# Kernel optimization log

Measured on AMD Instinct MI355X. Metric: run time of the kernel, lower is better.

The kernel has to match this reference:

```python
import jax, jax.numpy as jnp
import numpy as np

N = 4096      # nodes
E = 131072    # edges
C_IN = 128
HID = 128     # d_model of transformer (= embed_dim used in reshape_to_trans)
OUT = 32      # GNN output channels -> transformer seq_len
HEADS = 8
DH = HID // HEADS
FF = 2048     # torch TransformerEncoderLayer default dim_feedforward
EPS = 1e-5


def layer_norm(x, g, b):
    mu = jnp.mean(x, axis=-1, keepdims=True)
    var = jnp.mean(jnp.square(x - mu), axis=-1, keepdims=True)
    return (x - mu) * jax.lax.rsqrt(var + EPS) * g + b


def setup_inputs() -> dict:
    key = jax.random.key(0)
    ks = jax.random.split(key, 24)
    def rn(k, shape, scale=0.05):
        return jax.random.normal(k, shape, dtype=jnp.float32) * scale
    inp = {
        "x": jax.random.normal(ks[0], (N, C_IN), dtype=jnp.float32),
        "edge_index": jax.random.randint(ks[1], (2, E), 0, N, dtype=jnp.int64),
        # GCN layers
        "Wg1": rn(ks[2], (C_IN, HID)), "bg1": jnp.zeros((HID,), jnp.float32),
        "Wg2": rn(ks[3], (HID, HID)),  "bg2": jnp.zeros((HID,), jnp.float32),
        "Wg3": rn(ks[4], (HID, OUT)),  "bg3": jnp.zeros((OUT,), jnp.float32),
        # MHA
        "Wq": rn(ks[5], (HID, HID)), "bq": jnp.zeros((HID,), jnp.float32),
        "Wk": rn(ks[6], (HID, HID)), "bk": jnp.zeros((HID,), jnp.float32),
        "Wv": rn(ks[7], (HID, HID)), "bv": jnp.zeros((HID,), jnp.float32),
        "Wo": rn(ks[8], (HID, HID)), "bo": jnp.zeros((HID,), jnp.float32),
        "ln1_g": jnp.ones((HID,), jnp.float32), "ln1_b": jnp.zeros((HID,), jnp.float32),
        # FFN
        "W1": rn(ks[9], (HID, FF)),  "b1": jnp.zeros((FF,), jnp.float32),
        "W2": rn(ks[10], (FF, HID)), "b2": jnp.zeros((HID,), jnp.float32),
        "ln2_g": jnp.ones((HID,), jnp.float32), "ln2_b": jnp.zeros((HID,), jnp.float32),
    }
    return inp


def reference(x, edge_index, Wg1, bg1, Wg2, bg2, Wg3, bg3,
              Wq, bq, Wk, bk, Wv, bv, Wo, bo, ln1_g, ln1_b,
              W1, b1, W2, b2, ln2_g, ln2_b):
    # ---- GCN normalization (add self-loops, symmetric D^-1/2 (A+I) D^-1/2) ----
    loop = jnp.arange(N, dtype=edge_index.dtype)
    src = jnp.concatenate([edge_index[0], loop])
    dst = jnp.concatenate([edge_index[1], loop])
    deg = jax.ops.segment_sum(jnp.ones((E + N,), jnp.float32), dst, num_segments=N)
    dinv = jnp.where(deg > 0, jax.lax.rsqrt(deg), 0.0)
    norm = (dinv[src] * dinv[dst])[:, None]  # [E+N, 1]

    def gcn(h, W, b):
        m = h @ W                               # [N, d_out]
        agg = jax.ops.segment_sum(m[src] * norm, dst, num_segments=N)
        return agg + b

    h = jax.nn.relu(gcn(x, Wg1, bg1))
    h = jax.nn.relu(gcn(h, Wg2, bg2))
    h = jax.nn.relu(gcn(h, Wg3, bg3))           # [N, OUT]

    # ---- reshape_to_trans: [N, OUT] -> [N, OUT, HID] (repeat along embed dim) ----
    t = jnp.broadcast_to(h[:, :, None], (N, OUT, HID))

    # ---- TransformerEncoderLayer (post-norm, relu FFN, no dropout at eval) ----
    q = (t @ Wq + bq).reshape(N, OUT, HEADS, DH)
    k = (t @ Wk + bk).reshape(N, OUT, HEADS, DH)
    v = (t @ Wv + bv).reshape(N, OUT, HEADS, DH)
    scores = jnp.einsum("bqhd,bkhd->bhqk", q, k) / jnp.sqrt(jnp.float32(DH))
    attn = jax.nn.softmax(scores, axis=-1)
    ctx = jnp.einsum("bhqk,bkhd->bqhd", attn, v).reshape(N, OUT, HID)
    a = ctx @ Wo + bo
    x1 = layer_norm(t + a, ln1_g, ln1_b)
    f = jax.nn.relu(x1 @ W1 + b1) @ W2 + b2
    out = layer_norm(x1 + f, ln2_g, ln2_b)      # [N, OUT, HID]
    return out
```

## Files before the change

kernel.cpp:

```cpp
#include <hip/hip_runtime.h>

#define NN 4096
#define EE 131072
#define FFD 2048

typedef float f32x4 __attribute__((ext_vector_type(4)));
typedef __bf16 bf16x8 __attribute__((ext_vector_type(8)));
typedef unsigned int u32;
typedef u32 u32x4 __attribute__((ext_vector_type(4)));
typedef unsigned short u16;
typedef u16 u16x8 __attribute__((ext_vector_type(8)));

__device__ __forceinline__ u16 f2bf(float f) {
    unsigned u = __builtin_bit_cast(unsigned, f);
    return (u16)((u + 0x7FFFu + ((u >> 16) & 1u)) >> 16);
}
__device__ __forceinline__ float bf2f(u16 h) {
    unsigned u = ((unsigned)h) << 16;
    return __builtin_bit_cast(float, u);
}
__device__ __forceinline__ u32 cvtpk(float lo, float hi) {
    u32 r;
    asm("v_cvt_pk_bf16_f32 %0, %1, %2" : "=v"(r) : "v"(lo), "v"(hi));
    return r;
}

#define GLD16(g, l) __builtin_amdgcn_global_load_lds(                            \
    (const __attribute__((address_space(1))) void*)(g),                          \
    (__attribute__((address_space(3))) void*)(l), 16, 0, 0)

__device__ __forceinline__ int ldedge(const int* ei, int idx, int is64) {
    return is64 ? ei[2 * idx] : ei[idx];
}

__global__ void k_init(const int* __restrict__ ei, int* __restrict__ flag,
                       int* __restrict__ cnt) {
    if (blockIdx.x == 0) {
        if (threadIdx.x < 64) {
            int v = ei[2 * threadIdx.x + 1];
            unsigned long long any = __ballot(v != 0);
            if (threadIdx.x == 0) *flag = (any == 0ULL) ? 1 : 0;
        }
    } else {
        cnt[(blockIdx.x - 1) * 256 + threadIdx.x] = 0;
    }
}

__global__ void k_degi(const int* __restrict__ ei, const int* __restrict__ flag,
                       int* __restrict__ cnt) {
    int e = blockIdx.x * 256 + threadIdx.x;
    if (e >= EE) return;
    atomicAdd(&cnt[ldedge(ei, EE + e, *flag)], 1);
}
__global__ __launch_bounds__(1024) void k_scan(const int* __restrict__ cnt,
        int* __restrict__ rp, int* __restrict__ cur, float* __restrict__ dinv) {
    __shared__ int tsum[1024];
    int t = threadIdx.x;
    int c0 = cnt[t * 4], c1 = cnt[t * 4 + 1], c2 = cnt[t * 4 + 2], c3 = cnt[t * 4 + 3];
    int s = c0 + c1 + c2 + c3;
    tsum[t] = s;
    dinv[t * 4]     = rsqrtf((float)c0 + 1.0f);
    dinv[t * 4 + 1] = rsqrtf((float)c1 + 1.0f);
    dinv[t * 4 + 2] = rsqrtf((float)c2 + 1.0f);
    dinv[t * 4 + 3] = rsqrtf((float)c3 + 1.0f);
    __syncthreads();
    for (int off = 1; off < 1024; off <<= 1) {
        int v = (t >= off) ? tsum[t - off] : 0;
        __syncthreads();
        tsum[t] += v;
        __syncthreads();
    }
    int excl = tsum[t] - s;
    int p0 = excl, p1 = excl + c0, p2 = p1 + c1, p3 = p2 + c2;
    rp[t * 4] = p0; rp[t * 4 + 1] = p1; rp[t * 4 + 2] = p2; rp[t * 4 + 3] = p3;
    cur[t * 4] = p0; cur[t * 4 + 1] = p1; cur[t * 4 + 2] = p2; cur[t * 4 + 3] = p3;
    if (t == 1023) rp[4096] = excl + s;
}

__global__ __launch_bounds__(256) void k_fuse1(const int* __restrict__ ei,
        const int* __restrict__ flag, int* __restrict__ cur, int* __restrict__ es,
        const float* __restrict__ x, const float* __restrict__ Wg1,
        const float* __restrict__ dinv, float* __restrict__ ms,
        const float* __restrict__ W1, const float* __restrict__ W2,
        u16* __restrict__ w1t, u16* __restrict__ w2t,
        const float* __restrict__ Wq, const float* __restrict__ bq,
        const float* __restrict__ Wk, const float* __restrict__ bk,
        const float* __restrict__ Wv, const float* __restrict__ bv,
        const float* __restrict__ Wo, const float* __restrict__ bo,
        float* __restrict__ tc) {
    __shared__ float smem[64 * 65];
    int b = blockIdx.x, t = threadIdx.x;
    if (b < 512) {
        int e = b * 256 + t;
        int is64 = *flag;
        int s = ldedge(ei, e, is64), d = ldedge(ei, EE + e, is64);
        int pos = atomicAdd(&cur[d], 1);
        es[pos] = s;
    } else if (b < 2560) {
        int n0 = (b - 512) * 2, r = t >> 7, e = t & 127;
        smem[r * 128 + e] = x[(size_t)(n0 + r) * 128 + e];
        __syncthreads();
        float a = 0.f;
        #pragma unroll 8
        for (int c = 0; c < 128; ++c) a += smem[r * 128 + c] * Wg1[c * 128 + e];
        ms[(size_t)(n0 + r) * 128 + e] = a * dinv[n0 + r];
    } else if (b < 2624) {
        int bb = b - 2560;
        int c0 = (bb >> 5) * 64, f0 = (bb & 31) * 64;
        int rr = t >> 6, col = t & 63;
        #pragma unroll
        for (int k = 0; k < 16; ++k) {
            int row = k * 4 + rr;
            smem[row * 65 + col] = W1[(size_t)(c0 + row) * 2048 + f0 + col];
        }
        __syncthreads();
        #pragma unroll
        for (int k = 0; k < 16; ++k) {
            int frow = k * 4 + rr;
            w1t[(size_t)(f0 + frow) * 128 + c0 + col] = f2bf(smem[col * 65 + frow]);
        }
    } else if (b < 2688) {
        int bb = b - 2624;
        int f0 = (bb >> 1) * 64, o0 = (bb & 1) * 64;
        int rr = t >> 6, col = t & 63;
        #pragma unroll
        for (int k = 0; k < 16; ++k) {
            int row = k * 4 + rr;
            smem[row * 65 + col] = W2[(size_t)(f0 + row) * 128 + o0 + col];
        }
        __syncthreads();
        #pragma unroll
        for (int k = 0; k < 16; ++k) {
            int orow = k * 4 + rr;
            w2t[(size_t)(o0 + orow) * 2048 + f0 + col] = f2bf(smem[col * 65 + orow]);
        }
    } else {
        float aq = 0, ak = 0, av = 0;
        if (t < 128) {
            for (int c = 0; c < 128; ++c) {
                aq += Wq[c * 128 + t]; ak += Wk[c * 128 + t]; av += Wv[c * 128 + t];
            }
            smem[t] = aq; smem[128 + t] = ak; smem[256 + t] = av;
            tc[t] = aq; tc[128 + t] = ak; tc[256 + t] = av;
        }
        __syncthreads();
        if (t < 128) {
            float pb = 0;
            for (int d = 0; d < 128; ++d) pb += bv[d] * Wo[d * 128 + t];
            tc[1440 + t] = pb + bo[t];
            for (int hh = 0; hh < 8; ++hh) {
                float p = 0;
                #pragma unroll
                for (int d = hh * 16; d < hh * 16 + 16; ++d) p += smem[256 + d] * Wo[d * 128 + t];
                tc[416 + hh * 128 + t] = p;
            }
        }
        if (t < 8) {
            float A = 0, B = 0, C = 0, D = 0;
            #pragma unroll
            for (int d = t * 16; d < t * 16 + 16; ++d) {
                A += smem[d] * smem[128 + d]; B += smem[d] * bk[d];
                C += bq[d] * smem[128 + d];   D += bq[d] * bk[d];
            }
            tc[384 + t] = A; tc[392 + t] = B; tc[400 + t] = C; tc[408 + t] = D;
        }
    }
}

__global__ __launch_bounds__(256) void k_gcn_mm128(const float* __restrict__ h,
        const float* __restrict__ W, const float* __restrict__ dinv, float* __restrict__ ms) {
    __shared__ float hr[2][128];
    int t = threadIdx.x, n0 = blockIdx.x * 2, r = t >> 7, e = t & 127;
    hr[r][e] = h[(size_t)(n0 + r) * 128 + e];
    __syncthreads();
    float a = 0.f;
    #pragma unroll 8
    for (int c = 0; c < 128; ++c) a += hr[r][c] * W[c * 128 + e];
    ms[(size_t)(n0 + r) * 128 + e] = a * dinv[n0 + r];
}
__global__ __launch_bounds__(256) void k_gcn_mm32(const float* __restrict__ h,
        const float* __restrict__ W, const float* __restrict__ dinv, float* __restrict__ ms) {
    __shared__ float hr[8][128];
    int t = threadIdx.x, n0 = blockIdx.x * 8;
    for (int k2 = 0; k2 < 4; ++k2) {
        int idx = k2 * 256 + t;
        hr[idx >> 7][idx & 127] = h[(size_t)n0 * 128 + idx];
    }
    __syncthreads();
    int r = t >> 5, e = t & 31;
    float a = 0.f;
    #pragma unroll 8
    for (int c = 0; c < 128; ++c) a += hr[r][c] * W[c * 32 + e];
    ms[(size_t)(n0 + r) * 32 + e] = a * dinv[n0 + r];
}

__global__ __launch_bounds__(256) void k_gath128(const int* __restrict__ es,
        const int* __restrict__ rp, const float* __restrict__ ms,
        const float* __restrict__ dinv, const float* __restrict__ b,
        float* __restrict__ hout) {
    int node = blockIdx.x * 4 + (threadIdx.x >> 6), lane = threadIdx.x & 63;
    int st = rp[node], en = rp[node + 1];
    const float2* m2 = (const float2*)ms;
    float ax0 = 0.f, ay0 = 0.f, ax1 = 0.f, ay1 = 0.f;
    int e = st;
    for (; e + 2 <= en; e += 2) {
        int s0 = es[e], s1 = es[e + 1];
        float2 v0 = m2[(size_t)s0 * 64 + lane];
        float2 v1 = m2[(size_t)s1 * 64 + lane];
        ax0 += v0.x; ay0 += v0.y; ax1 += v1.x; ay1 += v1.y;
    }
    if (e < en) {
        float2 v = m2[(size_t)es[e] * 64 + lane];
        ax0 += v.x; ay0 += v.y;
    }
    float dv = dinv[node];
    float2 self = m2[(size_t)node * 64 + lane];
    int c = lane * 2;
    hout[(size_t)node * 128 + c]     = fmaxf(dv * (ax0 + ax1 + self.x) + b[c], 0.f);
    hout[(size_t)node * 128 + c + 1] = fmaxf(dv * (ay0 + ay1 + self.y) + b[c + 1], 0.f);
}

__global__ __launch_bounds__(256) void k_ga(const int* __restrict__ es,
        const int* __restrict__ rp, const float* __restrict__ ms,
        const float* __restrict__ dinv, const float* __restrict__ bg3,
        const float* __restrict__ tc, const float* __restrict__ g1,
        const float* __restrict__ b1n, u16* __restrict__ x1b) {
    __shared__ float sh[2][32];
    __shared__ float wsm[2][8][32];
    int b = blockIdx.x, t = threadIdx.x;
    int n0 = b * 2;
    if (t < 64) {
        int ni = t >> 5, sl = t & 31;
        int node = n0 + ni;
        int st = rp[node], en = rp[node + 1];
        float a0 = 0.f, a1 = 0.f;
        int e = st;
        for (; e + 2 <= en; e += 2) {
            a0 += ms[(size_t)es[e] * 32 + sl];
            a1 += ms[(size_t)es[e + 1] * 32 + sl];
        }
        if (e < en) a0 += ms[(size_t)es[e] * 32 + sl];
        float dv = dinv[node];
        sh[ni][sl] = fmaxf(dv * (a0 + a1 + ms[(size_t)node * 32 + sl]) + bg3[sl], 0.f);
    }
    __syncthreads();
    #pragma unroll
    for (int rep = 0; rep < 2; ++rep) {
        int idx = rep * 256 + t;
        int ni = idx >> 8, hh = (idx >> 5) & 7, i = idx & 31;
        float A = tc[384 + hh], C = tc[400 + hh];
        float coef = (sh[ni][i] * A + C) * 0.25f;
        float m = -1e30f;
        #pragma unroll
        for (int j = 0; j < 32; ++j) m = fmaxf(m, coef * sh[ni][j]);
        float s = 0.f, wsum = 0.f;
        #pragma unroll
        for (int j = 0; j < 32; ++j) {
            float e = __expf(coef * sh[ni][j] - m);
            s += e; wsum += e * sh[ni][j];
        }
        wsm[ni][hh][i] = wsum / s;
    }
    __syncthreads();
    int wave = t >> 6, lane = t & 63;
    int ni = wave >> 1;
    float pb0 = tc[1440 + lane], pb1 = tc[1440 + lane + 64];
    float po0[8], po1[8];
    #pragma unroll
    for (int hh = 0; hh < 8; ++hh) {
        po0[hh] = tc[416 + hh * 128 + lane];
        po1[hh] = tc[416 + hh * 128 + lane + 64];
    }
    float ga = g1[lane], gb = g1[lane + 64], ba = b1n[lane], bb = b1n[lane + 64];
    size_t nbase = (size_t)(n0 + ni) * 32;
    for (int i = (wave & 1); i < 32; i += 2) {
        float y0 = sh[ni][i] + pb0, y1 = sh[ni][i] + pb1;
        #pragma unroll
        for (int hh = 0; hh < 8; ++hh) {
            float w = wsm[ni][hh][i];
            y0 += w * po0[hh]; y1 += w * po1[hh];
        }
        float s1 = y0 + y1, s2 = y0 * y0 + y1 * y1;
        #pragma unroll
        for (int off = 1; off < 64; off <<= 1) {
            s1 += __shfl_xor(s1, off); s2 += __shfl_xor(s2, off);
        }
        float mu = s1 * (1.f / 128.f);
        float var = s2 * (1.f / 128.f) - mu * mu;
        float rs = rsqrtf(var + 1e-5f);
        size_t base = (nbase + i) * 128;
        x1b[base + lane]      = f2bf((y0 - mu) * rs * ga + ba);
        x1b[base + lane + 64] = f2bf((y1 - mu) * rs * gb + bb);
    }
}

#define STAGE32(buf, Fb) {                                                       \
    char* db_ = (char*)(buf);                                                    \
    _Pragma("unroll") for (int c1_ = 0; c1_ < 2; ++c1_) {                        \
        int f_ = c1_ * 16 + (t >> 4);                                            \
        int bo_ = ((t & 15) * 16) ^ ((f_ & 7) << 4);                             \
        GLD16(w1t + (size_t)((Fb) + f_) * 128 + (bo_ >> 1),                      \
              db_ + c1_ * 4096 + wave * 1024);                                   \
    }                                                                            \
    _Pragma("unroll") for (int c2_ = 0; c2_ < 2; ++c2_) {                        \
        int op_ = c2_ * 32 + wave * 8 + ((t >> 3) & 7);                          \
        int pb_ = (t & 7) ^ ((t >> 3) & 7);                                      \
        int o_  = op_ * 2 + (pb_ >> 2);                                          \
        GLD16(w2t + (size_t)o_ * 2048 + (Fb) + (pb_ & 3) * 8,                    \
              db_ + 8192 + c2_ * 4096 + wave * 1024);                            \
    } }

#define FCOMP32(buf, Fb) {                                                       \
    const char* wb_ = (const char*)(buf);                                        \
    bf16x8 w2f_[8];                                                              \
    _Pragma("unroll") for (int c2_ = 0; c2_ < 8; ++c2_)                          \
        w2f_[c2_] = *(const bf16x8*)(wb_ + 8192 + (c2_ * 8 + (li >> 1)) * 128 +  \
            ((((li & 1) * 64) + g * 16) ^ ((li >> 1) << 4)));                    \
    _Pragma("unroll") for (int cf_ = 0; cf_ < 2; ++cf_) {                        \
        bf16x8 w1f_[4];                                                          \
        _Pragma("unroll") for (int ks_ = 0; ks_ < 4; ++ks_)                      \
            w1f_[ks_] = *(const bf16x8*)(wb_ + (cf_ * 16 + li) * 256 +           \
                ((ks_ * 64 + g * 16) ^ ((li & 7) << 4)));                        \
        f32x4 a0_ = (f32x4){0.f, 0.f, 0.f, 0.f};                                 \
        f32x4 a1_ = (f32x4){0.f, 0.f, 0.f, 0.f};                                 \
        _Pragma("unroll") for (int ks_ = 0; ks_ < 4; ++ks_) {                    \
            a0_ = __builtin_amdgcn_mfma_f32_16x16x32_bf16(af[0][ks_], w1f_[ks_], a0_, 0, 0, 0); \
            a1_ = __builtin_amdgcn_mfma_f32_16x16x32_bf16(af[1][ks_], w1f_[ks_], a1_, 0, 0, 0); \
        }                                                                        \
        float bias_ = b1[(Fb) + cf_ * 16 + li];                                  \
        u32 pkA0 = cvtpk(fmaxf(a0_[0] + bias_, 0.f), fmaxf(a0_[1] + bias_, 0.f)); \
        u32 pkA1 = cvtpk(fmaxf(a0_[2] + bias_, 0.f), fmaxf(a0_[3] + bias_, 0.f)); \
        u32 pkB0 = cvtpk(fmaxf(a1_[0] + bias_, 0.f), fmaxf(a1_[1] + bias_, 0.f)); \
        u32 pkB1 = cvtpk(fmaxf(a1_[2] + bias_, 0.f), fmaxf(a1_[3] + bias_, 0.f)); \
        int rp0_ = g * 2, rp1_ = g * 2 + 1;                                      \
        int wl_ = (cf_ * 16 + li) * 2;                                           \
        *(u16*)(hwb + rp0_ * 128 + ((wl_) ^ (rp0_ << 4)))        = (u16)pkA0;    \
        *(u16*)(hwb + rp0_ * 128 + ((64 + wl_) ^ (rp0_ << 4)))   = (u16)(pkA0 >> 16); \
        *(u16*)(hwb + rp1_ * 128 + ((wl_) ^ (rp1_ << 4)))        = (u16)pkA1;    \
        *(u16*)(hwb + rp1_ * 128 + ((64 + wl_) ^ (rp1_ << 4)))   = (u16)(pkA1 >> 16); \
        *(u16*)(hwb + (8 + rp0_) * 128 + ((wl_) ^ (rp0_ << 4)))      = (u16)pkB0; \
        *(u16*)(hwb + (8 + rp0_) * 128 + ((64 + wl_) ^ (rp0_ << 4))) = (u16)(pkB0 >> 16); \
        *(u16*)(hwb + (8 + rp1_) * 128 + ((wl_) ^ (rp1_ << 4)))      = (u16)pkB1; \
        *(u16*)(hwb + (8 + rp1_) * 128 + ((64 + wl_) ^ (rp1_ << 4))) = (u16)(pkB1 >> 16); \
    }                                                                            \
    {                                                                            \
        bf16x8 a2_[2];                                                           \
        _Pragma("unroll") for (int rf_ = 0; rf_ < 2; ++rf_)                      \
            a2_[rf_] = *(const bf16x8*)(hwb + (rf_ * 8 + (li >> 1)) * 128 +      \
                ((((li & 1) * 64) + g * 16) ^ ((li >> 1) << 4)));                \
        _Pragma("unroll") for (int c2_ = 0; c2_ < 8; ++c2_) {                    \
            acc2[0][c2_] = __builtin_amdgcn_mfma_f32_16x16x32_bf16(a2_[0], w2f_[c2_], acc2[0][c2_], 0, 0, 0); \
            acc2[1][c2_] = __builtin_amdgcn_mfma_f32_16x16x32_bf16(a2_[1], w2f_[c2_], acc2[1][c2_], 0, 0, 0); \
        }                                                                        \
    } }

__global__ __launch_bounds__(256, 3) void k_ffn(const u16* __restrict__ x1b,
        const u16* __restrict__ w1t, const u16* __restrict__ w2t,
        const float* __restrict__ b1, const float* __restrict__ b2,
        const float* __restrict__ g2, const float* __restrict__ bt2, float* __restrict__ out) {
    __shared__ u16 wA[8192];
    __shared__ u16 wB[8192];
    __shared__ u16 hid[4][1024];
    int t = threadIdx.x, wave = t >> 6, lane = t & 63;
    int g = lane >> 4, li = lane & 15;
    size_t rowbase = (size_t)blockIdx.x * 128;
    char* hwb = (char*)&hid[wave][0];

    STAGE32(wA, 0);

    bf16x8 af[2][4];
    #pragma unroll
    for (int rf = 0; rf < 2; ++rf)
    #pragma unroll
    for (int ks = 0; ks < 4; ++ks)
        af[rf][ks] = *(const bf16x8*)(x1b +
            (rowbase + wave * 32 + rf * 16 + li) * 128 + ks * 32 + g * 8);

    f32x4 acc2[2][8];
    #pragma unroll
    for (int a = 0; a < 2; ++a)
    #pragma unroll
    for (int b = 0; b < 8; ++b) acc2[a][b] = (f32x4){0.f, 0.f, 0.f, 0.f};

    __syncthreads();

    for (int F = 0; F < FFD; F += 64) {
        STAGE32(wB, F + 32);
        FCOMP32(wA, F);
        __syncthreads();
        if (F + 64 < FFD) STAGE32(wA, F + 64);
        FCOMP32(wB, F + 32);
        __syncthreads();
    }

    #pragma unroll
    for (int rf = 0; rf < 2; ++rf)
    #pragma unroll
    for (int r = 0; r < 4; ++r) {
        int lrow = wave * 32 + rf * 16 + g * 4 + r;
        size_t grow = rowbase + lrow;
        float vals[8], s1 = 0.f, s2 = 0.f;
        #pragma unroll
        for (int cf2 = 0; cf2 < 8; ++cf2) {
            int col = cf2 * 16 + li;
            float xv = bf2f(x1b[grow * 128 + col]);
            float y = xv + acc2[rf][cf2][r] + b2[col];
            vals[cf2] = y; s1 += y; s2 += y * y;
        }
        #pragma unroll
        for (int m = 1; m < 16; m <<= 1) {
            s1 += __shfl_xor(s1, m); s2 += __shfl_xor(s2, m);
        }
        float mu = s1 * (1.f / 128.f);
        float var = s2 * (1.f / 128.f) - mu * mu;
        float rs = rsqrtf(var + 1e-5f);
        #pragma unroll
        for (int cf2 = 0; cf2 < 8; ++cf2) {
            int col = cf2 * 16 + li;
            out[grow * 128 + col] = (vals[cf2] - mu) * rs * g2[col] + bt2[col];
        }
    }
}

extern "C" void kernel_launch(void* const* d_in, const int* in_sizes, int n_in,
                              void* d_out, int out_size, void* d_ws, size_t ws_size,
                              hipStream_t stream) {
    const float* x   = (const float*)d_in[0];
    const int*   ei  = (const int*)d_in[1];
    const float *Wg1 = (const float*)d_in[2],  *bg1 = (const float*)d_in[3];
    const float *Wg2 = (const float*)d_in[4],  *bg2 = (const float*)d_in[5];
    const float *Wg3 = (const float*)d_in[6],  *bg3 = (const float*)d_in[7];
    const float *Wq  = (const float*)d_in[8],  *bq  = (const float*)d_in[9];
    const float *Wk  = (const float*)d_in[10], *bk  = (const float*)d_in[11];
    const float *Wv  = (const float*)d_in[12], *bv  = (const float*)d_in[13];
    const float *Wo  = (const float*)d_in[14], *bo  = (const float*)d_in[15];
    const float *g1  = (const float*)d_in[16], *b1n = (const float*)d_in[17];
    const float *W1  = (const float*)d_in[18], *b1  = (const float*)d_in[19];
    const float *W2  = (const float*)d_in[20], *b2  = (const float*)d_in[21];
    const float *g2  = (const float*)d_in[22], *bt2 = (const float*)d_in[23];

    char* ws = (char*)d_ws;
    int*   flag = (int*)(ws + 0);
    int*   cnt  = (int*)(ws + 4096);
    int*   rp   = (int*)(ws + 20480);
    int*   cur  = (int*)(ws + 40960);
    float* dinv = (float*)(ws + 57344);
    float* ms   = (float*)(ws + 73728);
    int*   es   = (int*)(ws + 2170880);
    float* hA   = (float*)(ws + 2695168);
    float* hB   = (float*)(ws + 4792320);
    float* tc   = (float*)(ws + 6889472);
    u16*   w1t  = (u16*)(ws + 6897664);
    u16*   w2t  = (u16*)(ws + 7421952);
    u16*   x1b  = (u16*)(ws + 8388608);
    float* out  = (float*)d_out;

    k_init<<<17, 256, 0, stream>>>(ei, flag, cnt);
    k_degi<<<512, 256, 0, stream>>>(ei, flag, cnt);
    k_scan<<<1, 1024, 0, stream>>>(cnt, rp, cur, dinv);

    k_fuse1<<<2689, 256, 0, stream>>>(ei, flag, cur, es, x, Wg1, dinv, ms,
                                      W1, W2, w1t, w2t,
                                      Wq, bq, Wk, bk, Wv, bv, Wo, bo, tc);

    k_gath128<<<1024, 256, 0, stream>>>(es, rp, ms, dinv, bg1, hA);
    k_gcn_mm128<<<2048, 256, 0, stream>>>(hA, Wg2, dinv, ms);
    k_gath128<<<1024, 256, 0, stream>>>(es, rp, ms, dinv, bg2, hB);
    k_gcn_mm32<<<512, 256, 0, stream>>>(hB, Wg3, dinv, ms);

    k_ga<<<2048, 256, 0, stream>>>(es, rp, ms, dinv, bg3, tc, g1, b1n, x1b);

    k_ffn<<<1024, 256, 0, stream>>>(x1b, w1t, w2t, b1, b2, g2, bt2, out);
}
```

Measured before the change: 285.7 us.

## Fuse GCN gather-aggregate with following dense matmul; raise FFN occupancy hint

Merges each GCN neighbor-gather kernel with the next layer's per-node matmul. The aggregated row is kept in shared memory and multiplied by W right away, which removes the intermediate hA/hB global buffers and two kernel launches. Ping-pong ms buffers (msA/msB) replace the single shared ms to avoid read/write aliasing. The FFN launch bound is also raised from 3 to 4 blocks per CU, which may force register spilling.

Result: slower. 775.1 us (+171.3%).

```diff
diff --git a/kernel.cpp b/kernel.cpp
--- a/kernel.cpp
+++ b/kernel.cpp
@@ -167,40 +167,16 @@
     }
 }
 
-__global__ __launch_bounds__(256) void k_gcn_mm128(const float* __restrict__ h,
-        const float* __restrict__ W, const float* __restrict__ dinv, float* __restrict__ ms) {
-    __shared__ float hr[2][128];
-    int t = threadIdx.x, n0 = blockIdx.x * 2, r = t >> 7, e = t & 127;
-    hr[r][e] = h[(size_t)(n0 + r) * 128 + e];
-    __syncthreads();
-    float a = 0.f;
-    #pragma unroll 8
-    for (int c = 0; c < 128; ++c) a += hr[r][c] * W[c * 128 + e];
-    ms[(size_t)(n0 + r) * 128 + e] = a * dinv[n0 + r];
-}
-__global__ __launch_bounds__(256) void k_gcn_mm32(const float* __restrict__ h,
-        const float* __restrict__ W, const float* __restrict__ dinv, float* __restrict__ ms) {
-    __shared__ float hr[8][128];
-    int t = threadIdx.x, n0 = blockIdx.x * 8;
-    for (int k2 = 0; k2 < 4; ++k2) {
-        int idx = k2 * 256 + t;
-        hr[idx >> 7][idx & 127] = h[(size_t)n0 * 128 + idx];
-    }
-    __syncthreads();
-    int r = t >> 5, e = t & 31;
-    float a = 0.f;
-    #pragma unroll 8
-    for (int c = 0; c < 128; ++c) a += hr[r][c] * W[c * 32 + e];
-    ms[(size_t)(n0 + r) * 32 + e] = a * dinv[n0 + r];
-}
-
-__global__ __launch_bounds__(256) void k_gath128(const int* __restrict__ es,
-        const int* __restrict__ rp, const float* __restrict__ ms,
-        const float* __restrict__ dinv, const float* __restrict__ b,
-        float* __restrict__ hout) {
-    int node = blockIdx.x * 4 + (threadIdx.x >> 6), lane = threadIdx.x & 63;
+__global__ __launch_bounds__(256) void k_gm2(const int* __restrict__ es,
+        const int* __restrict__ rp, const float* __restrict__ msA,
+        const float* __restrict__ dinv, const float* __restrict__ bg,
+        const float* __restrict__ W, float* __restrict__ msB) {
+    __shared__ float sh[4][128];
+    int t = threadIdx.x, n0 = blockIdx.x * 4;
+    int wv = t >> 6, lane = t & 63;
+    int node = n0 + wv;
+    const float2* m2 = (const float2*)msA;
     int st = rp[node], en = rp[node + 1];
-    const float2* m2 = (const float2*)ms;
     float ax0 = 0.f, ay0 = 0.f, ax1 = 0.f, ay1 = 0.f;
     int e = st;
     for (; e + 2 <= en; e += 2) {
@@ -216,8 +192,55 @@
     float dv = dinv[node];
     float2 self = m2[(size_t)node * 64 + lane];
     int c = lane * 2;
-    hout[(size_t)node * 128 + c]     = fmaxf(dv * (ax0 + ax1 + self.x) + b[c], 0.f);
-    hout[(size_t)node * 128 + c + 1] = fmaxf(dv * (ay0 + ay1 + self.y) + b[c + 1], 0.f);
+    sh[wv][c]     = fmaxf(dv * (ax0 + ax1 + self.x) + bg[c], 0.f);
+    sh[wv][c + 1] = fmaxf(dv * (ay0 + ay1 + self.y) + bg[c + 1], 0.f);
+    __syncthreads();
+    int e2 = t & 127;
+    #pragma unroll
+    for (int p = 0; p < 2; ++p) {
+        int ni = p * 2 + (t >> 7);
+        float a = 0.f;
+        #pragma unroll 8
+        for (int cc = 0; cc < 128; ++cc) a += sh[ni][cc] * W[cc * 128 + e2];
+        msB[(size_t)(n0 + ni) * 128 + e2] = a * dinv[n0 + ni];
+    }
+}
+
+__global__ __launch_bounds__(256) void k_gm3(const int* __restrict__ es,
+        const int* __restrict__ rp, const float* __restrict__ msB,
+        const float* __restrict__ dinv, const float* __restrict__ bg,
+        const float* __restrict__ W, float* __restrict__ ms32) {
+    __shared__ float sh[4][128];
+    int t = threadIdx.x, n0 = blockIdx.x * 4;
+    int wv = t >> 6, lane = t & 63;
+    int node = n0 + wv;
+    const float2* m2 = (const float2*)msB;
+    int st = rp[node], en = rp[node + 1];
+    float ax0 = 0.f, ay0 = 0.f, ax1 = 0.f, ay1 = 0.f;
+    int e = st;
+    for (; e + 2 <= en; e += 2) {
+        int s0 = es[e], s1 = es[e + 1];
+        float2 v0 = m2[(size_t)s0 * 64 + lane];
+        float2 v1 = m2[(size_t)s1 * 64 + lane];
+        ax0 += v0.x; ay0 += v0.y; ax1 += v1.x; ay1 += v1.y;
+    }
+    if (e < en) {
+        float2 v = m2[(size_t)es[e] * 64 + lane];
+        ax0 += v.x; ay0 += v.y;
+    }
+    float dv = dinv[node];
+    float2 self = m2[(size_t)node * 64 + lane];
+    int c = lane * 2;
+    sh[wv][c]     = fmaxf(dv * (ax0 + ax1 + self.x) + bg[c], 0.f);
+    sh[wv][c + 1] = fmaxf(dv * (ay0 + ay1 + self.y) + bg[c + 1], 0.f);
+    __syncthreads();
+    if (t < 128) {
+        int ni = t >> 5, e2 = t & 31;
+        float a = 0.f;
+        #pragma unroll 8
+        for (int cc = 0; cc < 128; ++cc) a += sh[ni][cc] * W[cc * 32 + e2];
+        ms32[(size_t)(n0 + ni) * 32 + e2] = a * dinv[n0 + ni];
+    }
 }
 
 __global__ __launch_bounds__(256) void k_ga(const int* __restrict__ es,
@@ -354,7 +377,7 @@
         }                                                                        \
     } }
 
-__global__ __launch_bounds__(256, 3) void k_ffn(const u16* __restrict__ x1b,
+__global__ __launch_bounds__(256, 4) void k_ffn(const u16* __restrict__ x1b,
         const u16* __restrict__ w1t, const u16* __restrict__ w2t,
         const float* __restrict__ b1, const float* __restrict__ b2,
         const float* __restrict__ g2, const float* __restrict__ bt2, float* __restrict__ out) {
@@ -445,30 +468,28 @@
     int*   rp   = (int*)(ws + 20480);
     int*   cur  = (int*)(ws + 40960);
     float* dinv = (float*)(ws + 57344);
-    float* ms   = (float*)(ws + 73728);
+    float* msA  = (float*)(ws + 73728);
     int*   es   = (int*)(ws + 2170880);
-    float* hA   = (float*)(ws + 2695168);
-    float* hB   = (float*)(ws + 4792320);
+    float* msB  = (float*)(ws + 2695168);
     float* tc   = (float*)(ws + 6889472);
     u16*   w1t  = (u16*)(ws + 6897664);
     u16*   w2t  = (u16*)(ws + 7421952);
     u16*   x1b  = (u16*)(ws + 8388608);
+    float* ms32 = msA;
     float* out  = (float*)d_out;
 
     k_init<<<17, 256, 0, stream>>>(ei, flag, cnt);
     k_degi<<<512, 256, 0, stream>>>(ei, flag, cnt);
     k_scan<<<1, 1024, 0, stream>>>(cnt, rp, cur, dinv);
 
-    k_fuse1<<<2689, 256, 0, stream>>>(ei, flag, cur, es, x, Wg1, dinv, ms,
+    k_fuse1<<<2689, 256, 0, stream>>>(ei, flag, cur, es, x, Wg1, dinv, msA,
                                       W1, W2, w1t, w2t,
                                       Wq, bq, Wk, bk, Wv, bv, Wo, bo, tc);
 
-    k_gath128<<<1024, 256, 0, stream>>>(es, rp, ms, dinv, bg1, hA);
-    k_gcn_mm128<<<2048, 256, 0, stream>>>(hA, Wg2, dinv, ms);
-    k_gath128<<<1024, 256, 0, stream>>>(es, rp, ms, dinv, bg2, hB);
-    k_gcn_mm32<<<512, 256, 0, stream>>>(hB, Wg3, dinv, ms);
-
-    k_ga<<<2048, 256, 0, stream>>>(es, rp, ms, dinv, bg3, tc, g1, b1n, x1b);
+    k_gm2<<<1024, 256, 0, stream>>>(es, rp, msA, dinv, bg1, Wg2, msB);
+    k_gm3<<<1024, 256, 0, stream>>>(es, rp, msB, dinv, bg2, Wg3, ms32);
+
+    k_ga<<<2048, 256, 0, stream>>>(es, rp, ms32, dinv, bg3, tc, g1, b1n, x1b);
 
     k_ffn<<<1024, 256, 0, stream>>>(x1b, w1t, w2t, b1, b2, g2, bt2, out);
 }
```
